# Optimization experiments

Hardware: AMD Instinct MI355X
Metric: run time of the kernel (lower is better)

Reference implementation:

```python
import jax, jax.numpy as jnp
import numpy as np

V = 128   # vocab_size
H = 1024  # rnn_hidden_size
L = 2     # rnn_num_layers
B = 64    # batch
T = 256   # seq_len


def setup_inputs() -> dict:
    key = jax.random.key(0)
    ks = jax.random.split(key, 1 + 4 * L)
    inp = {"x": jax.random.randint(ks[0], (B, T), 0, V)}
    s = 1.0 / np.sqrt(H)  # torch GRU init range
    k = 1
    for l in range(L):
        in_dim = V if l == 0 else 2 * H
        inp[f"Wih{l}"] = jax.random.uniform(ks[k], (2, 3 * H, in_dim), minval=-s, maxval=s); k += 1
        inp[f"Whh{l}"] = jax.random.uniform(ks[k], (2, 3 * H, H), minval=-s, maxval=s); k += 1
        inp[f"bih{l}"] = jax.random.uniform(ks[k], (2, 3 * H), minval=-s, maxval=s); k += 1
        inp[f"bhh{l}"] = jax.random.uniform(ks[k], (2, 3 * H), minval=-s, maxval=s); k += 1
    return inp


def _gru_dir(x_seq, Wih, Whh, bih, bhh, reverse):
    # x_seq: [B, T, in_dim]; Wih: [3H, in_dim]; Whh: [3H, H]
    xp = jnp.einsum('bti,gi->btg', x_seq, Wih) + bih  # batched input projection
    if reverse:
        xp = xp[:, ::-1]
    h0 = jnp.zeros((x_seq.shape[0], H), x_seq.dtype)

    def step(h, xpt):
        g = h @ Whh.T + bhh
        xr, xz, xn = jnp.split(xpt, 3, axis=-1)
        hr, hz, hn = jnp.split(g, 3, axis=-1)
        r = jax.nn.sigmoid(xr + hr)
        z = jax.nn.sigmoid(xz + hz)
        n = jnp.tanh(xn + r * hn)
        h_new = (1.0 - z) * n + z * h
        return h_new, h_new

    hT, ys = jax.lax.scan(step, h0, jnp.swapaxes(xp, 0, 1))  # scan over time
    ys = jnp.swapaxes(ys, 0, 1)  # [B, T, H]
    if reverse:
        ys = ys[:, ::-1]
    return ys, hT


def _encoder(x, params):
    inp_seq = jax.nn.one_hot(x, V, dtype=jnp.float32)  # [B, T, V]
    hiddens = []
    for (Wih, Whh, bih, bhh) in params:
        yf, hf = _gru_dir(inp_seq, Wih[0], Whh[0], bih[0], bhh[0], False)
        yb, hb = _gru_dir(inp_seq, Wih[1], Whh[1], bih[1], bhh[1], True)
        inp_seq = jnp.concatenate([yf, yb], axis=-1)  # [B, T, 2H]
        hiddens += [hf, hb]
    return inp_seq, jnp.stack(hiddens)  # ([B,T,2H], [2L,B,H])


def reference(x, Wih0, Whh0, bih0, bhh0, Wih1, Whh1, bih1, bhh1):
    params = [(Wih0, Whh0, bih0, bhh0), (Wih1, Whh1, bih1, bhh1)]
    return _encoder(x, params)
```

## Files before the change

### kernel.cpp

```cpp
#include <hip/hip_runtime.h>
#include <stdint.h>
#include <math.h>


#define B_  64
#define T_  256
#define H_  1024
#define G3_ 3072

#define SW_BYTES (3 * 32 * 64 * 16)
#define SX_ROW 132
#define SMEM_BYTES (SW_BYTES + 48 * SX_ROW * 4)

typedef __attribute__((ext_vector_type(8))) __bf16 bf16x8;
typedef __attribute__((ext_vector_type(4))) float  f32x4;

union FragU { uint4 u; bf16x8 b; };

__device__ __forceinline__ float bf2f(unsigned short v) {
  return __builtin_bit_cast(float, (uint32_t)v << 16);
}
__device__ __forceinline__ unsigned short f2bf(float f) {
  uint32_t u = __builtin_bit_cast(uint32_t, f);
  u += 0x7FFFu + ((u >> 16) & 1u);
  return (unsigned short)(u >> 16);
}

__device__ __forceinline__ float sigm_fast(float x) {
  x = fminf(fmaxf(x, -60.f), 60.f);
  return 1.f / (1.f + __expf(-x));
}
__device__ __forceinline__ float tanh_fast(float x) {
  const float xc = fminf(fmaxf(x, -15.f), 15.f);
  const float e = __expf(2.f * xc);
  return (e - 1.f) / (e + 1.f);
}

__device__ __forceinline__ void bar_arrive_wait(unsigned* bar, unsigned k) {
  unsigned* sub = bar + 32u * (1u + (blockIdx.x & 7u));
  bool rel = false;
  if (__hip_atomic_fetch_add(sub, 1u, __ATOMIC_RELAXED, __HIP_MEMORY_SCOPE_AGENT)
      == 16u * k - 1u) {
    if (__hip_atomic_fetch_add(bar, 1u, __ATOMIC_RELAXED, __HIP_MEMORY_SCOPE_AGENT)
        == 8u * k - 1u) {
      __hip_atomic_store(bar + 384, k, __ATOMIC_RELAXED, __HIP_MEMORY_SCOPE_AGENT);
      rel = true;
    }
  }
  if (!rel) {
    unsigned spins = 0;
    while (__hip_atomic_load(bar + 384, __ATOMIC_RELAXED, __HIP_MEMORY_SCOPE_AGENT) < k) {
      __builtin_amdgcn_s_sleep(4);
      if (++spins > (1u << 20)) break;
    }
  }
}

__global__ void detect_dtype(const unsigned short* __restrict__ p, int* __restrict__ flag) {
  const int i = threadIdx.x;
  const unsigned short v = p[2 * i];
  const int e = (v >> 7) & 0xFF;
  const unsigned long long m = __ballot(e <= 124);
  if (i == 0) *flag = (m == ~0ull) ? 1 : 0;
}

__device__ __forceinline__ float load_canon(const void* src, int i, bool isbf) {
  return isbf ? bf2f(((const unsigned short*)src)[i]) : ((const float*)src)[i];
}

__global__ void prep_split(const void* __restrict__ src, int n,
                           unsigned short* __restrict__ hi, unsigned short* __restrict__ lo,
                           const int* __restrict__ flag) {
  const int i = blockIdx.x * blockDim.x + threadIdx.x;
  if (i >= n) return;
  const bool isbf = (*flag != 0);
  const float f = load_canon(src, i, isbf);
  const unsigned short h = f2bf(f);
  hi[i] = h;
  lo[i] = f2bf(f - bf2f(h));
}

__global__ void prep_f32(const void* __restrict__ src, int n,
                         float* __restrict__ dst, const int* __restrict__ flag) {
  const int i = blockIdx.x * blockDim.x + threadIdx.x;
  if (i >= n) return;
  const bool isbf = (*flag != 0);
  dst[i] = load_canon(src, i, isbf);
}

#define LD2(K, OFF)                                                         \
  asm volatile("global_load_dwordx4 %0, %2, off offset:" OFF " sc0 sc1\n\t" \
               "global_load_dwordx4 %1, %3, off offset:" OFF " sc0 sc1"     \
               : "=&v"(ah[K].u), "=&v"(al[K].u)                             \
               : "v"(aph), "v"(apl));

#define STH(P, V)                                                 \
  asm volatile("global_store_short %0, %1, off sc0 sc1"           \
               :: "v"(P), "v"(V) : "memory");

template<int LAYER>
__global__ __launch_bounds__(128, 1) void gru_scan(
    const int*            __restrict__ x,
    const float*          __restrict__ Wih0f,
    const float*          __restrict__ bihf,
    const _Float16*       __restrict__ xp1,
    const unsigned short* __restrict__ WhhH,
    const unsigned short* __restrict__ WhhL,
    const float*          __restrict__ bhhf,
    unsigned short*       __restrict__ hhi,
    unsigned short*       __restrict__ hlo,
    unsigned short*       __restrict__ ys0_hi,
    unsigned short*       __restrict__ ys0_lo,
    void*                 __restrict__ d_out,
    const int*            __restrict__ flag,
    unsigned*             __restrict__ bar_mem)
{
  extern __shared__ unsigned char smem[];
  unsigned short* sW = (unsigned short*)smem;
  float*          sX = (float*)(smem + SW_BYTES);

  const int j0   = blockIdx.x << 4;
  const int d    = blockIdx.y;
  const int bh   = blockIdx.z;
  const int tid  = threadIdx.x;
  const int w    = tid >> 6;
  const int lane = tid & 63;
  const int quad = lane >> 4, l15 = lane & 15;
  const bool out_bf = (*flag != 0);
  const bool wlo    = (*flag == 0);

  const int j = j0 + l15;
  const size_t HF_HALF = (size_t)2 * B_ * H_;

  {
    const unsigned short* base = WhhH + (size_t)d * G3_ * H_;
    for (int idx = tid; idx < 48 * 128; idx += 128) {
      const int row = idx >> 7;
      const int c16 = idx & 127;
      const int g = row >> 4, u = row & 15;
      const int kt = c16 >> 2, q = c16 & 3;
      const uint4 v = *(const uint4*)(base + (size_t)(g * H_ + j0 + u) * H_ + (c16 << 3));
      *(uint4*)&sW[(((g << 5) + kt) << 9) + (((q << 4) + u) << 3)] = v;
    }
  }
  if (LAYER == 0) {
    const float* W0 = Wih0f + (size_t)d * G3_ * 128;
    for (int idx = tid; idx < 48 * 32; idx += 128) {
      const int row = idx >> 5, c = (idx & 31) << 2;
      const int g = row >> 4, u = row & 15;
      const float4 v = *(const float4*)(W0 + (size_t)(g * H_ + j0 + u) * 128 + c);
      *(float4*)&sX[row * SX_ROW + c] = v;
    }
  }
  __syncthreads();

  const int am = (bh << 5) + (w << 4) + l15;
  const int bb = (bh << 5) + (w << 4) + (quad << 2);
  const unsigned short *aphS[2], *aplS[2];
  unsigned short *hhiS[2], *hloS[2];
#pragma unroll
  for (int s = 0; s < 2; ++s) {
    aphS[s] = hhi + s * HF_HALF + ((size_t)d * B_ + am) * H_ + (quad << 3);
    aplS[s] = hlo + s * HF_HALF + ((size_t)d * B_ + am) * H_ + (quad << 3);
    hhiS[s] = hhi + s * HF_HALF + (size_t)d * B_ * H_;
    hloS[s] = hlo + s * HF_HALF + (size_t)d * B_ * H_;
  }

  const unsigned short* bplG[3];
#pragma unroll
  for (int g = 0; g < 3; ++g)
    bplG[g] = WhhL + (size_t)d * G3_ * H_ + (size_t)(g * H_ + j) * H_ + (quad << 3);

  const size_t dj = (size_t)d * G3_ + j;
  const float bhr = bhhf[dj];
  const float bhz = bhhf[dj + H_];
  const float bhn = bhhf[dj + 2 * H_];
  float bir = 0.f, biz = 0.f, bin_ = 0.f;
  const float *sXr = nullptr, *sXz = nullptr, *sXn = nullptr;
  if (LAYER == 0) {
    bir  = bihf[dj];
    biz  = bihf[dj + H_];
    bin_ = bihf[dj + 2 * H_];
    sXr = sX + (size_t)l15 * SX_ROW;
    sXz = sX + (size_t)(16 + l15) * SX_ROW;
    sXn = sX + (size_t)(32 + l15) * SX_ROW;
  }
  const _Float16* xpd = (LAYER == 1) ? (xp1 + (size_t)d * (B_ * T_) * G3_) : nullptr;

  float*          out_f  = (float*)d_out;
  unsigned short* out_b  = (unsigned short*)d_out;
  const size_t    HIDOFF = (size_t)B_ * T_ * 2048;

  unsigned* bar = bar_mem + (size_t)d * 1024;
  float hprev[4] = {0.f, 0.f, 0.f, 0.f};

  if (!wlo) {
    float xr[4], xz[4], xn[4];
    _Float16 xph[12];
    {
      const int te = d ? (T_ - 1) : 0;
      if (LAYER == 0) {
#pragma unroll
        for (int r = 0; r < 4; ++r) {
          const int tok = x[(bb + r) * T_ + te];
          xr[r] = sXr[tok] + bir; xz[r] = sXz[tok] + biz; xn[r] = sXn[tok] + bin_;
        }
      } else {
#pragma unroll
        for (int r = 0; r < 4; ++r) {
          const _Float16* xpb = xpd + ((size_t)(bb + r) * T_ + te) * G3_;
          xph[r * 3 + 0] = xpb[j]; xph[r * 3 + 1] = xpb[j + H_]; xph[r * 3 + 2] = xpb[j + 2 * H_];
        }
      }
    }

    for (int t = 0; t < T_; ++t) {
      const int t_eff = d ? (T_ - 1 - t) : t;
      const int pi = t & 1, po = pi ^ 1;
      const unsigned short* aph = aphS[pi];
      const unsigned short* apl = aplS[pi];

      FragU ah[32], al[32];
      LD2(0, "0")    LD2(1, "64")   LD2(2, "128")  LD2(3, "192")
      LD2(4, "256")  LD2(5, "320")  LD2(6, "384")  LD2(7, "448")
      LD2(8, "512")  LD2(9, "576")  LD2(10, "640") LD2(11, "704")
      LD2(12, "768") LD2(13, "832") LD2(14, "896") LD2(15, "960")
      LD2(16, "1024") LD2(17, "1088") LD2(18, "1152") LD2(19, "1216")
      LD2(20, "1280") LD2(21, "1344") LD2(22, "1408") LD2(23, "1472")
      LD2(24, "1536") LD2(25, "1600") LD2(26, "1664") LD2(27, "1728")
      LD2(28, "1792") LD2(29, "1856") LD2(30, "1920") LD2(31, "1984")

      f32x4 acc[3] = {};
      asm volatile("s_waitcnt vmcnt(32)" ::: "memory");
      __builtin_amdgcn_sched_barrier(0);
#pragma unroll
      for (int kt = 0; kt < 16; ++kt) {
        FragU f0, f1, f2;
        f0.u = *(const uint4*)(sW + ((kt      ) << 9) + (lane << 3));
        f1.u = *(const uint4*)(sW + ((kt +  32) << 9) + (lane << 3));
        f2.u = *(const uint4*)(sW + ((kt +  64) << 9) + (lane << 3));
        acc[0] = __builtin_amdgcn_mfma_f32_16x16x32_bf16(ah[kt].b, f0.b, acc[0], 0, 0, 0);
        acc[0] = __builtin_amdgcn_mfma_f32_16x16x32_bf16(al[kt].b, f0.b, acc[0], 0, 0, 0);
        acc[1] = __builtin_amdgcn_mfma_f32_16x16x32_bf16(ah[kt].b, f1.b, acc[1], 0, 0, 0);
        acc[1] = __builtin_amdgcn_mfma_f32_16x16x32_bf16(al[kt].b, f1.b, acc[1], 0, 0, 0);
        acc[2] = __builtin_amdgcn_mfma_f32_16x16x32_bf16(ah[kt].b, f2.b, acc[2], 0, 0, 0);
        acc[2] = __builtin_amdgcn_mfma_f32_16x16x32_bf16(al[kt].b, f2.b, acc[2], 0, 0, 0);
      }
      asm volatile("s_waitcnt vmcnt(0)" ::: "memory");
      __builtin_amdgcn_sched_barrier(0);
#pragma unroll
      for (int kt = 16; kt < 32; ++kt) {
        FragU f0, f1, f2;
        f0.u = *(const uint4*)(sW + ((kt      ) << 9) + (lane << 3));
        f1.u = *(const uint4*)(sW + ((kt +  32) << 9) + (lane << 3));
        f2.u = *(const uint4*)(sW + ((kt +  64) << 9) + (lane << 3));
        acc[0] = __builtin_amdgcn_mfma_f32_16x16x32_bf16(ah[kt].b, f0.b, acc[0], 0, 0, 0);
        acc[0] = __builtin_amdgcn_mfma_f32_16x16x32_bf16(al[kt].b, f0.b, acc[0], 0, 0, 0);
        acc[1] = __builtin_amdgcn_mfma_f32_16x16x32_bf16(ah[kt].b, f1.b, acc[1], 0, 0, 0);
        acc[1] = __builtin_amdgcn_mfma_f32_16x16x32_bf16(al[kt].b, f1.b, acc[1], 0, 0, 0);
        acc[2] = __builtin_amdgcn_mfma_f32_16x16x32_bf16(ah[kt].b, f2.b, acc[2], 0, 0, 0);
        acc[2] = __builtin_amdgcn_mfma_f32_16x16x32_bf16(al[kt].b, f2.b, acc[2], 0, 0, 0);
      }

      if (LAYER == 1) {
#pragma unroll
        for (int r = 0; r < 4; ++r) {
          xr[r] = (float)xph[r * 3 + 0];
          xz[r] = (float)xph[r * 3 + 1];
          xn[r] = (float)xph[r * 3 + 2];
        }
      }

      unsigned short* pHi = hhiS[po] + (size_t)bb * H_ + j;
      unsigned short* pLo = hloS[po] + (size_t)bb * H_ + j;
#pragma unroll
      for (int r = 0; r < 4; ++r) {
        const int b = bb + r;
        const float gr = acc[0][r] + bhr;
        const float gz = acc[1][r] + bhz;
        const float gn = acc[2][r] + bhn;
        const float rg = sigm_fast(xr[r] + gr);
        const float zg = sigm_fast(xz[r] + gz);
        const float ng = tanh_fast(xn[r] + rg * gn);
        const float hnew = (1.f - zg) * ng + zg * hprev[r];
        hprev[r] = hnew;

        const unsigned short hi = f2bf(hnew);
        const unsigned short lo = f2bf(hnew - bf2f(hi));
        STH(pHi + (size_t)r * H_, (uint32_t)hi);
        STH(pLo + (size_t)r * H_, (uint32_t)lo);

        const size_t yoff = ((size_t)b * T_ + t_eff) * 2048 + d * H_ + j;
        if (LAYER == 0) {
          ys0_hi[yoff] = hi;
          ys0_lo[yoff] = lo;
        } else {
          if (out_bf) out_b[yoff] = hi; else out_f[yoff] = hnew;
        }
        if (t == T_ - 1) {
          const size_t hh = HIDOFF + ((size_t)(LAYER * 2 + d) * B_ + b) * H_ + j;
          if (out_bf) out_b[hh] = hi; else out_f[hh] = hnew;
        }
      }

      if (t + 1 < T_) {
        asm volatile("s_waitcnt vmcnt(0)" ::: "memory");
        __syncthreads();
        const int te = d ? (T_ - 2 - t) : (t + 1);
        if (LAYER == 0) {
#pragma unroll
          for (int r = 0; r < 4; ++r) {
            const int tok = x[(bb + r) * T_ + te];
            xr[r] = sXr[tok] + bir; xz[r] = sXz[tok] + biz; xn[r] = sXn[tok] + bin_;
          }
        } else {
#pragma unroll
          for (int r = 0; r < 4; ++r) {
            const _Float16* xpb = xpd + ((size_t)(bb + r) * T_ + te) * G3_;
            xph[r * 3 + 0] = xpb[j]; xph[r * 3 + 1] = xpb[j + H_]; xph[r * 3 + 2] = xpb[j + 2 * H_];
          }
        }
        if (tid == 0) bar_arrive_wait(bar, (unsigned)(t + 1));
        __syncthreads();
      }
    }
  } else {
    for (int t = 0; t < T_; ++t) {
      const int t_eff = d ? (T_ - 1 - t) : t;
      const int pi = t & 1, po = pi ^ 1;

      float xr[4], xz[4], xn[4];
      if (LAYER == 0) {
#pragma unroll
        for (int r = 0; r < 4; ++r) {
          const int tok = x[(bb + r) * T_ + t_eff];
          xr[r] = sXr[tok] + bir; xz[r] = sXz[tok] + biz; xn[r] = sXn[tok] + bin_;
        }
      } else {
#pragma unroll
        for (int r = 0; r < 4; ++r) {
          const _Float16* xpb = xpd + ((size_t)(bb + r) * T_ + t_eff) * G3_;
          xr[r] = (float)xpb[j]; xz[r] = (float)xpb[j + H_]; xn[r] = (float)xpb[j + 2 * H_];
        }
      }

      const unsigned short* aph = aphS[pi];
      const unsigned short* apl = aplS[pi];
      f32x4 acc[3] = {};
#pragma unroll
      for (int kt = 0; kt < 32; ++kt) {
        FragU ah, al;
        ah.u = *(const uint4*)(aph + (kt << 5));
        al.u = *(const uint4*)(apl + (kt << 5));
#pragma unroll
        for (int g = 0; g < 3; ++g) {
          FragU fb, fl;
          fb.u = *(const uint4*)(sW + (((g << 5) + kt) << 9) + (lane << 3));
          fl.u = *(const uint4*)(bplG[g] + (kt << 5));
          acc[g] = __builtin_amdgcn_mfma_f32_16x16x32_bf16(ah.b, fb.b, acc[g], 0, 0, 0);
          acc[g] = __builtin_amdgcn_mfma_f32_16x16x32_bf16(al.b, fb.b, acc[g], 0, 0, 0);
          acc[g] = __builtin_amdgcn_mfma_f32_16x16x32_bf16(ah.b, fl.b, acc[g], 0, 0, 0);
        }
      }

#pragma unroll
      for (int r = 0; r < 4; ++r) {
        const int b = bb + r;
        const float gr = acc[0][r] + bhr;
        const float gz = acc[1][r] + bhz;
        const float gn = acc[2][r] + bhn;
        const float rg = 1.f / (1.f + expf(-(xr[r] + gr)));
        const float zg = 1.f / (1.f + expf(-(xz[r] + gz)));
        const float ng = tanhf(xn[r] + rg * gn);
        const float hnew = (1.f - zg) * ng + zg * hprev[r];
        hprev[r] = hnew;

        const size_t ho = (size_t)b * H_ + j;
        const unsigned short hi = f2bf(hnew);
        const unsigned short lo = f2bf(hnew - bf2f(hi));
        hhiS[po][ho] = hi;
        hloS[po][ho] = lo;

        const size_t yoff = ((size_t)b * T_ + t_eff) * 2048 + d * H_ + j;
        if (LAYER == 0) {
          ys0_hi[yoff] = hi;
          ys0_lo[yoff] = lo;
        } else {
          if (out_bf) out_b[yoff] = hi; else out_f[yoff] = hnew;
        }
        if (t == T_ - 1) {
          const size_t hh = HIDOFF + ((size_t)(LAYER * 2 + d) * B_ + b) * H_ + j;
          if (out_bf) out_b[hh] = hi; else out_f[hh] = hnew;
        }
      }

      if (t + 1 < T_) {
        __syncthreads();
        if (tid == 0) {
          __builtin_amdgcn_fence(__ATOMIC_RELEASE, "agent");
          bar_arrive_wait(bar, (unsigned)(t + 1));
          __builtin_amdgcn_fence(__ATOMIC_ACQUIRE, "agent");
        }
        __syncthreads();
      }
    }
  }
}

__global__ __launch_bounds__(256) void xp1_gemm(
    const unsigned short* __restrict__ Ahi,
    const unsigned short* __restrict__ Alo,
    const unsigned short* __restrict__ Bhi,
    const unsigned short* __restrict__ Blo,
    const float*          __restrict__ biasf,
    _Float16*             __restrict__ xp1,
    const int*            __restrict__ flag)
{
  const int nt  = blockIdx.x;
  const int mt  = blockIdx.y;
  const int d   = blockIdx.z;
  const int tid = threadIdx.x;
  const int w = tid >> 6, lane = tid & 63;
  const int quad = lane >> 4, l15 = lane & 15;
  const int wm = w >> 1, wn = w & 1;
  const bool wlo = (*flag == 0);

  __shared__ unsigned short sAh[128][40];
  __shared__ unsigned short sAl[128][40];
  __shared__ unsigned short sBh[128][40];
  __shared__ unsigned short sBl[128][40];

  const int srow = tid >> 1;
  const int scol = (tid & 1) << 4;
  const unsigned short* gAh = Ahi + (size_t)(mt * 128 + srow) * 2048 + scol;
  const unsigned short* gAl = Alo + (size_t)(mt * 128 + srow) * 2048 + scol;
  const unsigned short* gBh = Bhi + (size_t)d * G3_ * 2048
                                  + (size_t)(nt * 128 + srow) * 2048 + scol;
  const unsigned short* gBl = Blo + (size_t)d * G3_ * 2048
                                  + (size_t)(nt * 128 + srow) * 2048 + scol;

  f32x4 acc[4][4] = {};

  for (int k0 = 0; k0 < 2048; k0 += 32) {
    const uint4 a0 = *(const uint4*)(gAh + k0);
    const uint4 a1 = *(const uint4*)(gAh + k0 + 8);
    const uint4 l0 = *(const uint4*)(gAl + k0);
    const uint4 l1 = *(const uint4*)(gAl + k0 + 8);
    const uint4 b0 = *(const uint4*)(gBh + k0);
    const uint4 b1 = *(const uint4*)(gBh + k0 + 8);
    uint4 c0, c1;
    if (wlo) { c0 = *(const uint4*)(gBl + k0); c1 = *(const uint4*)(gBl + k0 + 8); }
    __syncthreads();
    *(uint4*)&sAh[srow][scol]     = a0;
    *(uint4*)&sAh[srow][scol + 8] = a1;
    *(uint4*)&sAl[srow][scol]     = l0;
    *(uint4*)&sAl[srow][scol + 8] = l1;
    *(uint4*)&sBh[srow][scol]     = b0;
    *(uint4*)&sBh[srow][scol + 8] = b1;
    if (wlo) {
      *(uint4*)&sBl[srow][scol]     = c0;
      *(uint4*)&sBl[srow][scol + 8] = c1;
    }
    __syncthreads();

    bf16x8 fah[4], fal[4], fbh[4];
#pragma unroll
    for (int i = 0; i < 4; ++i) {
      FragU fa; fa.u = *(const uint4*)&sAh[(wm << 6) + (i << 4) + l15][quad << 3]; fah[i] = fa.b;
      FragU fl; fl.u = *(const uint4*)&sAl[(wm << 6) + (i << 4) + l15][quad << 3]; fal[i] = fl.b;
      FragU fb; fb.u = *(const uint4*)&sBh[(wn << 6) + (i << 4) + l15][quad << 3]; fbh[i] = fb.b;
    }
#pragma unroll
    for (int i = 0; i < 4; ++i)
#pragma unroll
      for (int jj = 0; jj < 4; ++jj) {
        acc[i][jj] = __builtin_amdgcn_mfma_f32_16x16x32_bf16(fah[i], fbh[jj], acc[i][jj], 0, 0, 0);
        acc[i][jj] = __builtin_amdgcn_mfma_f32_16x16x32_bf16(fal[i], fbh[jj], acc[i][jj], 0, 0, 0);
      }
    if (wlo) {
#pragma unroll
      for (int jj = 0; jj < 4; ++jj) {
        FragU fc; fc.u = *(const uint4*)&sBl[(wn << 6) + (jj << 4) + l15][quad << 3];
#pragma unroll
        for (int i = 0; i < 4; ++i)
          acc[i][jj] = __builtin_amdgcn_mfma_f32_16x16x32_bf16(fah[i], fc.b, acc[i][jj], 0, 0, 0);
      }
    }
  }

#pragma unroll
  for (int jj = 0; jj < 4; ++jj) {
    const int col = nt * 128 + (wn << 6) + (jj << 4) + l15;
    const float bias = biasf[(size_t)d * G3_ + col];
#pragma unroll
    for (int i = 0; i < 4; ++i) {
      const int m = mt * 128 + (wm << 6) + (i << 4) + (quad << 2);
      _Float16* op = xp1 + ((size_t)d * (B_ * T_) + m) * G3_ + col;
#pragma unroll
      for (int r = 0; r < 4; ++r) op[(size_t)r * G3_] = (_Float16)(acc[i][jj][r] + bias);
    }
  }
}

extern "C" void kernel_launch(void* const* d_in, const int* in_sizes, int n_in,
                              void* d_out, int out_size, void* d_ws, size_t ws_size,
                              hipStream_t stream)
{
  const int*  x    = (const int*)d_in[0];
  const void* Wih0 = d_in[1];
  const void* Whh0 = d_in[2];
  const void* bih0 = d_in[3];
  const void* bhh0 = d_in[4];
  const void* Wih1 = d_in[5];
  const void* Whh1 = d_in[6];
  const void* bih1 = d_in[7];
  const void* bhh1 = d_in[8];

  const size_t FLAG_B = 256;
  const size_t XP1_B  = (size_t)2 * B_ * T_ * G3_ * 2;
  const size_t YS_B   = (size_t)B_ * T_ * 2048 * 2;
  const size_t WHH_B  = (size_t)2 * G3_ * H_ * 2;
  const size_t WIH1_B = (size_t)2 * G3_ * 2048 * 2;
  const size_t WIH0_B = (size_t)2 * G3_ * 128 * 4;
  const size_t BIAS_B = (size_t)2 * G3_ * 4;
  const size_t HB_B   = (size_t)2 * 2 * B_ * H_ * 2;
  const size_t BAR_B  = 8192;
  const size_t NEED = FLAG_B + XP1_B + 2 * YS_B + 4 * WHH_B + 2 * WIH1_B
                    + WIH0_B + 4 * BIAS_B + 2 * HB_B + BAR_B;
  if (ws_size < NEED) return;

  char* p = (char*)d_ws;
  int*            flag    = (int*)p;            p += FLAG_B;
  _Float16*       xp1     = (_Float16*)p;       p += XP1_B;
  unsigned short* ys0_hi  = (unsigned short*)p; p += YS_B;
  unsigned short* ys0_lo  = (unsigned short*)p; p += YS_B;
  unsigned short* Whh0H   = (unsigned short*)p; p += WHH_B;
  unsigned short* Whh0L   = (unsigned short*)p; p += WHH_B;
  unsigned short* Whh1H   = (unsigned short*)p; p += WHH_B;
  unsigned short* Whh1L   = (unsigned short*)p; p += WHH_B;
  unsigned short* Wih1H   = (unsigned short*)p; p += WIH1_B;
  unsigned short* Wih1L   = (unsigned short*)p; p += WIH1_B;
  float*          Wih0f   = (float*)p;          p += WIH0_B;
  float*          bih0f   = (float*)p;          p += BIAS_B;
  float*          bhh0f   = (float*)p;          p += BIAS_B;
  float*          bih1f   = (float*)p;          p += BIAS_B;
  float*          bhh1f   = (float*)p;          p += BIAS_B;
  char*           hbase   = p;
  unsigned short* hhi     = (unsigned short*)hbase;
  unsigned short* hlo     = (unsigned short*)(hbase + HB_B);
  unsigned*       bar     = (unsigned*)(hbase + 2 * HB_B);

  hipFuncSetAttribute((const void*)&gru_scan<0>,
                      hipFuncAttributeMaxDynamicSharedMemorySize, SMEM_BYTES);
  hipFuncSetAttribute((const void*)&gru_scan<1>,
                      hipFuncAttributeMaxDynamicSharedMemorySize, SMEM_BYTES);

  detect_dtype<<<1, 64, 0, stream>>>((const unsigned short*)bih0, flag);

  const int NWHH  = 2 * G3_ * H_;
  const int NWIH1 = 2 * G3_ * 2048;
  const int NWIH0 = 2 * G3_ * 128;
  const int NBIAS = 2 * G3_;
  prep_split<<<(NWHH  + 255) / 256, 256, 0, stream>>>(Whh0, NWHH,  Whh0H, Whh0L, flag);
  prep_split<<<(NWHH  + 255) / 256, 256, 0, stream>>>(Whh1, NWHH,  Whh1H, Whh1L, flag);
  prep_split<<<(NWIH1 + 255) / 256, 256, 0, stream>>>(Wih1, NWIH1, Wih1H, Wih1L, flag);
  prep_f32<<<(NWIH0 + 255) / 256, 256, 0, stream>>>(Wih0, NWIH0, Wih0f, flag);
  prep_f32<<<(NBIAS + 255) / 256, 256, 0, stream>>>(bih0, NBIAS, bih0f, flag);
  prep_f32<<<(NBIAS + 255) / 256, 256, 0, stream>>>(bhh0, NBIAS, bhh0f, flag);
  prep_f32<<<(NBIAS + 255) / 256, 256, 0, stream>>>(bih1, NBIAS, bih1f, flag);
  prep_f32<<<(NBIAS + 255) / 256, 256, 0, stream>>>(bhh1, NBIAS, bhh1f, flag);

  hipMemsetAsync(hbase, 0, 2 * HB_B + BAR_B, stream);
  gru_scan<0><<<dim3(64, 2, 2), 128, SMEM_BYTES, stream>>>(
      x, Wih0f, bih0f, nullptr, Whh0H, Whh0L, bhh0f,
      hhi, hlo, ys0_hi, ys0_lo, d_out, flag, bar);

  xp1_gemm<<<dim3(24, 128, 2), 256, 0, stream>>>(ys0_hi, ys0_lo, Wih1H, Wih1L, bih1f, xp1, flag);

  hipMemsetAsync(hbase, 0, 2 * HB_B + BAR_B, stream);
  gru_scan<1><<<dim3(64, 2, 2), 128, SMEM_BYTES, stream>>>(
      x, nullptr, nullptr, xp1, Whh1H, Whh1L, bhh1f,
      hhi, hlo, nullptr, nullptr, d_out, flag, bar);
}
```

Baseline: 12.49 ms.

## Replace atomic counter barrier with per-group flag barrier and pack hidden hi/lo words

Replaces the per-direction two-level atomic fetch-add barrier with a flag-based barrier. Each block publishes its step count to a padded flag, a leader block ballots over all 64 flags and then releases per-group go flags, and barriers are now scoped per (direction, batch-half) group rather than per direction. The hidden state's bf16 hi and lo parts are interleaved into one 32-bit word, so each element is one dword store and one load stream instead of two, with perm instructions unpacking them before the MFMAs. It also moves the layer-0 token-embedding lookup after the matmul so the token load overlaps the barrier. This adds a leader hop and larger barrier memory, and the polling latency of the leader could dominate.

```diff
diff --git a/kernel.cpp b/kernel.cpp
--- a/kernel.cpp
+++ b/kernel.cpp
@@ -36,24 +36,16 @@
   return (e - 1.f) / (e + 1.f);
 }
 
-__device__ __forceinline__ void bar_arrive_wait(unsigned* bar, unsigned k) {
-  unsigned* sub = bar + 32u * (1u + (blockIdx.x & 7u));
-  bool rel = false;
-  if (__hip_atomic_fetch_add(sub, 1u, __ATOMIC_RELAXED, __HIP_MEMORY_SCOPE_AGENT)
-      == 16u * k - 1u) {
-    if (__hip_atomic_fetch_add(bar, 1u, __ATOMIC_RELAXED, __HIP_MEMORY_SCOPE_AGENT)
-        == 8u * k - 1u) {
-      __hip_atomic_store(bar + 384, k, __ATOMIC_RELAXED, __HIP_MEMORY_SCOPE_AGENT);
-      rel = true;
-    }
-  }
-  if (!rel) {
-    unsigned spins = 0;
-    while (__hip_atomic_load(bar + 384, __ATOMIC_RELAXED, __HIP_MEMORY_SCOPE_AGENT) < k) {
-      __builtin_amdgcn_s_sleep(4);
-      if (++spins > (1u << 20)) break;
-    }
-  }
+__device__ __forceinline__ void unpack2(const FragU& q0, const FragU& q1,
+                                        FragU& ah, FragU& al) {
+  ah.u.x = __builtin_amdgcn_perm(q0.u.y, q0.u.x, 0x05040100u);
+  ah.u.y = __builtin_amdgcn_perm(q0.u.w, q0.u.z, 0x05040100u);
+  ah.u.z = __builtin_amdgcn_perm(q1.u.y, q1.u.x, 0x05040100u);
+  ah.u.w = __builtin_amdgcn_perm(q1.u.w, q1.u.z, 0x05040100u);
+  al.u.x = __builtin_amdgcn_perm(q0.u.y, q0.u.x, 0x07060302u);
+  al.u.y = __builtin_amdgcn_perm(q0.u.w, q0.u.z, 0x07060302u);
+  al.u.z = __builtin_amdgcn_perm(q1.u.y, q1.u.x, 0x07060302u);
+  al.u.w = __builtin_amdgcn_perm(q1.u.w, q1.u.z, 0x07060302u);
 }
 
 __global__ void detect_dtype(const unsigned short* __restrict__ p, int* __restrict__ flag) {
@@ -88,14 +80,14 @@
   dst[i] = load_canon(src, i, isbf);
 }
 
-#define LD2(K, OFF)                                                         \
-  asm volatile("global_load_dwordx4 %0, %2, off offset:" OFF " sc0 sc1\n\t" \
-               "global_load_dwordx4 %1, %3, off offset:" OFF " sc0 sc1"     \
-               : "=&v"(ah[K].u), "=&v"(al[K].u)                             \
-               : "v"(aph), "v"(apl));
-
-#define STH(P, V)                                                 \
-  asm volatile("global_store_short %0, %1, off sc0 sc1"           \
+#define LDP(K, O0, O1)                                                      \
+  asm volatile("global_load_dwordx4 %0, %2, off offset:" O0 " sc0 sc1\n\t"  \
+               "global_load_dwordx4 %1, %2, off offset:" O1 " sc0 sc1"      \
+               : "=&v"(p0[K].u), "=&v"(p1[K].u)                             \
+               : "v"(ap32));
+
+#define STW(P, V)                                                 \
+  asm volatile("global_store_dword %0, %1, off sc0 sc1"           \
                :: "v"(P), "v"(V) : "memory");
 
 template<int LAYER>
@@ -107,8 +99,7 @@
     const unsigned short* __restrict__ WhhH,
     const unsigned short* __restrict__ WhhL,
     const float*          __restrict__ bhhf,
-    unsigned short*       __restrict__ hhi,
-    unsigned short*       __restrict__ hlo,
+    unsigned*             __restrict__ h32,
     unsigned short*       __restrict__ ys0_hi,
     unsigned short*       __restrict__ ys0_lo,
     void*                 __restrict__ d_out,
@@ -128,6 +119,7 @@
   const int quad = lane >> 4, l15 = lane & 15;
   const bool out_bf = (*flag != 0);
   const bool wlo    = (*flag == 0);
+  const bool leader = (blockIdx.x == 0);
 
   const int j = j0 + l15;
   const size_t HF_HALF = (size_t)2 * B_ * H_;
@@ -156,14 +148,12 @@
 
   const int am = (bh << 5) + (w << 4) + l15;
   const int bb = (bh << 5) + (w << 4) + (quad << 2);
-  const unsigned short *aphS[2], *aplS[2];
-  unsigned short *hhiS[2], *hloS[2];
+  const unsigned *ap32S[2];
+  unsigned *h32S[2];
 #pragma unroll
   for (int s = 0; s < 2; ++s) {
-    aphS[s] = hhi + s * HF_HALF + ((size_t)d * B_ + am) * H_ + (quad << 3);
-    aplS[s] = hlo + s * HF_HALF + ((size_t)d * B_ + am) * H_ + (quad << 3);
-    hhiS[s] = hhi + s * HF_HALF + (size_t)d * B_ * H_;
-    hloS[s] = hlo + s * HF_HALF + (size_t)d * B_ * H_;
+    ap32S[s] = h32 + s * HF_HALF + ((size_t)d * B_ + am) * H_ + (quad << 3);
+    h32S[s]  = h32 + s * HF_HALF + (size_t)d * B_ * H_;
   }
 
   const unsigned short* bplG[3];
@@ -191,20 +181,17 @@
   unsigned short* out_b  = (unsigned short*)d_out;
   const size_t    HIDOFF = (size_t)B_ * T_ * 2048;
 
-  unsigned* bar = bar_mem + (size_t)d * 1024;
+  unsigned* grp = bar_mem + (size_t)(d * 2 + bh) * 72 * 1024;
   float hprev[4] = {0.f, 0.f, 0.f, 0.f};
 
   if (!wlo) {
-    float xr[4], xz[4], xn[4];
+    int ptok[4];
     _Float16 xph[12];
     {
       const int te = d ? (T_ - 1) : 0;
       if (LAYER == 0) {
 #pragma unroll
-        for (int r = 0; r < 4; ++r) {
-          const int tok = x[(bb + r) * T_ + te];
-          xr[r] = sXr[tok] + bir; xz[r] = sXz[tok] + biz; xn[r] = sXn[tok] + bin_;
-        }
+        for (int r = 0; r < 4; ++r) ptok[r] = x[(bb + r) * T_ + te];
       } else {
 #pragma unroll
         for (int r = 0; r < 4; ++r) {
@@ -217,52 +204,63 @@
     for (int t = 0; t < T_; ++t) {
       const int t_eff = d ? (T_ - 1 - t) : t;
       const int pi = t & 1, po = pi ^ 1;
-      const unsigned short* aph = aphS[pi];
-      const unsigned short* apl = aplS[pi];
-
-      FragU ah[32], al[32];
-      LD2(0, "0")    LD2(1, "64")   LD2(2, "128")  LD2(3, "192")
-      LD2(4, "256")  LD2(5, "320")  LD2(6, "384")  LD2(7, "448")
-      LD2(8, "512")  LD2(9, "576")  LD2(10, "640") LD2(11, "704")
-      LD2(12, "768") LD2(13, "832") LD2(14, "896") LD2(15, "960")
-      LD2(16, "1024") LD2(17, "1088") LD2(18, "1152") LD2(19, "1216")
-      LD2(20, "1280") LD2(21, "1344") LD2(22, "1408") LD2(23, "1472")
-      LD2(24, "1536") LD2(25, "1600") LD2(26, "1664") LD2(27, "1728")
-      LD2(28, "1792") LD2(29, "1856") LD2(30, "1920") LD2(31, "1984")
+      const unsigned* ap32 = ap32S[pi];
+
+      FragU p0[32], p1[32];
+      LDP(0, "0", "16")        LDP(1, "128", "144")    LDP(2, "256", "272")
+      LDP(3, "384", "400")     LDP(4, "512", "528")    LDP(5, "640", "656")
+      LDP(6, "768", "784")     LDP(7, "896", "912")    LDP(8, "1024", "1040")
+      LDP(9, "1152", "1168")   LDP(10, "1280", "1296") LDP(11, "1408", "1424")
+      LDP(12, "1536", "1552")  LDP(13, "1664", "1680") LDP(14, "1792", "1808")
+      LDP(15, "1920", "1936")  LDP(16, "2048", "2064") LDP(17, "2176", "2192")
+      LDP(18, "2304", "2320")  LDP(19, "2432", "2448") LDP(20, "2560", "2576")
+      LDP(21, "2688", "2704")  LDP(22, "2816", "2832") LDP(23, "2944", "2960")
+      LDP(24, "3072", "3088")  LDP(25, "3200", "3216") LDP(26, "3328", "3344")
+      LDP(27, "3456", "3472")  LDP(28, "3584", "3600") LDP(29, "3712", "3728")
+      LDP(30, "3840", "3856")  LDP(31, "3968", "3984")
 
       f32x4 acc[3] = {};
       asm volatile("s_waitcnt vmcnt(32)" ::: "memory");
       __builtin_amdgcn_sched_barrier(0);
 #pragma unroll
       for (int kt = 0; kt < 16; ++kt) {
-        FragU f0, f1, f2;
+        FragU ah, al, f0, f1, f2;
+        unpack2(p0[kt], p1[kt], ah, al);
         f0.u = *(const uint4*)(sW + ((kt      ) << 9) + (lane << 3));
         f1.u = *(const uint4*)(sW + ((kt +  32) << 9) + (lane << 3));
         f2.u = *(const uint4*)(sW + ((kt +  64) << 9) + (lane << 3));
-        acc[0] = __builtin_amdgcn_mfma_f32_16x16x32_bf16(ah[kt].b, f0.b, acc[0], 0, 0, 0);
-        acc[0] = __builtin_amdgcn_mfma_f32_16x16x32_bf16(al[kt].b, f0.b, acc[0], 0, 0, 0);
-        acc[1] = __builtin_amdgcn_mfma_f32_16x16x32_bf16(ah[kt].b, f1.b, acc[1], 0, 0, 0);
-        acc[1] = __builtin_amdgcn_mfma_f32_16x16x32_bf16(al[kt].b, f1.b, acc[1], 0, 0, 0);
-        acc[2] = __builtin_amdgcn_mfma_f32_16x16x32_bf16(ah[kt].b, f2.b, acc[2], 0, 0, 0);
-        acc[2] = __builtin_amdgcn_mfma_f32_16x16x32_bf16(al[kt].b, f2.b, acc[2], 0, 0, 0);
+        acc[0] = __builtin_amdgcn_mfma_f32_16x16x32_bf16(ah.b, f0.b, acc[0], 0, 0, 0);
+        acc[0] = __builtin_amdgcn_mfma_f32_16x16x32_bf16(al.b, f0.b, acc[0], 0, 0, 0);
+        acc[1] = __builtin_amdgcn_mfma_f32_16x16x32_bf16(ah.b, f1.b, acc[1], 0, 0, 0);
+        acc[1] = __builtin_amdgcn_mfma_f32_16x16x32_bf16(al.b, f1.b, acc[1], 0, 0, 0);
+        acc[2] = __builtin_amdgcn_mfma_f32_16x16x32_bf16(ah.b, f2.b, acc[2], 0, 0, 0);
+        acc[2] = __builtin_amdgcn_mfma_f32_16x16x32_bf16(al.b, f2.b, acc[2], 0, 0, 0);
       }
       asm volatile("s_waitcnt vmcnt(0)" ::: "memory");
       __builtin_amdgcn_sched_barrier(0);
 #pragma unroll
       for (int kt = 16; kt < 32; ++kt) {
-        FragU f0, f1, f2;
+        FragU ah, al, f0, f1, f2;
+        unpack2(p0[kt], p1[kt], ah, al);
         f0.u = *(const uint4*)(sW + ((kt      ) << 9) + (lane << 3));
         f1.u = *(const uint4*)(sW + ((kt +  32) << 9) + (lane << 3));
         f2.u = *(const uint4*)(sW + ((kt +  64) << 9) + (lane << 3));
-        acc[0] = __builtin_amdgcn_mfma_f32_16x16x32_bf16(ah[kt].b, f0.b, acc[0], 0, 0, 0);
-        acc[0] = __builtin_amdgcn_mfma_f32_16x16x32_bf16(al[kt].b, f0.b, acc[0], 0, 0, 0);
-        acc[1] = __builtin_amdgcn_mfma_f32_16x16x32_bf16(ah[kt].b, f1.b, acc[1], 0, 0, 0);
-        acc[1] = __builtin_amdgcn_mfma_f32_16x16x32_bf16(al[kt].b, f1.b, acc[1], 0, 0, 0);
-        acc[2] = __builtin_amdgcn_mfma_f32_16x16x32_bf16(ah[kt].b, f2.b, acc[2], 0, 0, 0);
-        acc[2] = __builtin_amdgcn_mfma_f32_16x16x32_bf16(al[kt].b, f2.b, acc[2], 0, 0, 0);
-      }
-
-      if (LAYER == 1) {
+        acc[0] = __builtin_amdgcn_mfma_f32_16x16x32_bf16(ah.b, f0.b, acc[0], 0, 0, 0);
+        acc[0] = __builtin_amdgcn_mfma_f32_16x16x32_bf16(al.b, f0.b, acc[0], 0, 0, 0);
+        acc[1] = __builtin_amdgcn_mfma_f32_16x16x32_bf16(ah.b, f1.b, acc[1], 0, 0, 0);
+        acc[1] = __builtin_amdgcn_mfma_f32_16x16x32_bf16(al.b, f1.b, acc[1], 0, 0, 0);
+        acc[2] = __builtin_amdgcn_mfma_f32_16x16x32_bf16(ah.b, f2.b, acc[2], 0, 0, 0);
+        acc[2] = __builtin_amdgcn_mfma_f32_16x16x32_bf16(al.b, f2.b, acc[2], 0, 0, 0);
+      }
+
+      float xr[4], xz[4], xn[4];
+      if (LAYER == 0) {
+#pragma unroll
+        for (int r = 0; r < 4; ++r) {
+          const int tok = ptok[r];
+          xr[r] = sXr[tok] + bir; xz[r] = sXz[tok] + biz; xn[r] = sXn[tok] + bin_;
+        }
+      } else {
 #pragma unroll
         for (int r = 0; r < 4; ++r) {
           xr[r] = (float)xph[r * 3 + 0];
@@ -271,8 +269,7 @@
         }
       }
 
-      unsigned short* pHi = hhiS[po] + (size_t)bb * H_ + j;
-      unsigned short* pLo = hloS[po] + (size_t)bb * H_ + j;
+      unsigned* pW = h32S[po] + (size_t)bb * H_ + j;
 #pragma unroll
       for (int r = 0; r < 4; ++r) {
         const int b = bb + r;
@@ -287,8 +284,8 @@
 
         const unsigned short hi = f2bf(hnew);
         const unsigned short lo = f2bf(hnew - bf2f(hi));
-        STH(pHi + (size_t)r * H_, (uint32_t)hi);
-        STH(pLo + (size_t)r * H_, (uint32_t)lo);
+        const unsigned hv = (unsigned)hi | ((unsigned)lo << 16);
+        STW(pW + (size_t)r * H_, hv);
 
         const size_t yoff = ((size_t)b * T_ + t_eff) * 2048 + d * H_ + j;
         if (LAYER == 0) {
@@ -304,15 +301,16 @@
       }
 
       if (t + 1 < T_) {
+        const unsigned k = (unsigned)(t + 1);
         asm volatile("s_waitcnt vmcnt(0)" ::: "memory");
         __syncthreads();
+        if (tid == 0)
+          __hip_atomic_store(grp + (unsigned)blockIdx.x * 1024u, k,
+                             __ATOMIC_RELAXED, __HIP_MEMORY_SCOPE_AGENT);
         const int te = d ? (T_ - 2 - t) : (t + 1);
         if (LAYER == 0) {
 #pragma unroll
-          for (int r = 0; r < 4; ++r) {
-            const int tok = x[(bb + r) * T_ + te];
-            xr[r] = sXr[tok] + bir; xz[r] = sXz[tok] + biz; xn[r] = sXn[tok] + bin_;
-          }
+          for (int r = 0; r < 4; ++r) ptok[r] = x[(bb + r) * T_ + te];
         } else {
 #pragma unroll
           for (int r = 0; r < 4; ++r) {
@@ -320,7 +318,29 @@
             xph[r * 3 + 0] = xpb[j]; xph[r * 3 + 1] = xpb[j + H_]; xph[r * 3 + 2] = xpb[j + 2 * H_];
           }
         }
-        if (tid == 0) bar_arrive_wait(bar, (unsigned)(t + 1));
+        if (leader) {
+          if (tid < 64) {
+            unsigned* fl = grp + (unsigned)tid * 1024u;
+            unsigned spins = 0;
+            for (;;) {
+              const unsigned v = __hip_atomic_load(fl, __ATOMIC_RELAXED, __HIP_MEMORY_SCOPE_AGENT);
+              if (__ballot(v >= k) == ~0ull) break;
+              __builtin_amdgcn_s_sleep(1);
+              if (++spins > (1u << 20)) break;
+            }
+            if (tid < 8)
+              __hip_atomic_store(grp + (64u + (unsigned)tid) * 1024u, k,
+                                 __ATOMIC_RELAXED, __HIP_MEMORY_SCOPE_AGENT);
+          }
+        } else if (tid == 0) {
+          unsigned* gl = grp + (64u + ((unsigned)blockIdx.x & 7u)) * 1024u;
+          unsigned spins = 0;
+          while (__hip_atomic_load(gl, __ATOMIC_RELAXED, __HIP_MEMORY_SCOPE_AGENT) < k) {
+            if (spins < 8) __builtin_amdgcn_s_sleep(1);
+            else           __builtin_amdgcn_s_sleep(8);
+            if (++spins > (1u << 20)) break;
+          }
+        }
         __syncthreads();
       }
     }
@@ -344,14 +364,14 @@
         }
       }
 
-      const unsigned short* aph = aphS[pi];
-      const unsigned short* apl = aplS[pi];
+      const unsigned* ap32 = ap32S[pi];
       f32x4 acc[3] = {};
 #pragma unroll
       for (int kt = 0; kt < 32; ++kt) {
-        FragU ah, al;
-        ah.u = *(const uint4*)(aph + (kt << 5));
-        al.u = *(const uint4*)(apl + (kt << 5));
+        FragU q0, q1, ah, al;
+        q0.u = *(const uint4*)(ap32 + (kt << 5));
+        q1.u = *(const uint4*)(ap32 + (kt << 5) + 4);
+        unpack2(q0, q1, ah, al);
 #pragma unroll
         for (int g = 0; g < 3; ++g) {
           FragU fb, fl;
@@ -363,6 +383,7 @@
         }
       }
 
+      unsigned* pW = h32S[po] + (size_t)bb * H_ + j;
 #pragma unroll
       for (int r = 0; r < 4; ++r) {
         const int b = bb + r;
@@ -375,11 +396,9 @@
         const float hnew = (1.f - zg) * ng + zg * hprev[r];
         hprev[r] = hnew;
 
-        const size_t ho = (size_t)b * H_ + j;
         const unsigned short hi = f2bf(hnew);
         const unsigned short lo = f2bf(hnew - bf2f(hi));
-        hhiS[po][ho] = hi;
-        hloS[po][ho] = lo;
+        pW[(size_t)r * H_] = (unsigned)hi | ((unsigned)lo << 16);
 
         const size_t yoff = ((size_t)b * T_ + t_eff) * 2048 + d * H_ + j;
         if (LAYER == 0) {
@@ -395,12 +414,37 @@
       }
 
       if (t + 1 < T_) {
+        const unsigned k = (unsigned)(t + 1);
         __syncthreads();
         if (tid == 0) {
           __builtin_amdgcn_fence(__ATOMIC_RELEASE, "agent");
-          bar_arrive_wait(bar, (unsigned)(t + 1));
-          __builtin_amdgcn_fence(__ATOMIC_ACQUIRE, "agent");
-        }
+          __hip_atomic_store(grp + (unsigned)blockIdx.x * 1024u, k,
+                             __ATOMIC_RELAXED, __HIP_MEMORY_SCOPE_AGENT);
+        }
+        if (leader) {
+          if (tid < 64) {
+            unsigned* fl = grp + (unsigned)tid * 1024u;
+            unsigned spins = 0;
+            for (;;) {
+              const unsigned v = __hip_atomic_load(fl, __ATOMIC_RELAXED, __HIP_MEMORY_SCOPE_AGENT);
+              if (__ballot(v >= k) == ~0ull) break;
+              __builtin_amdgcn_s_sleep(4);
+              if (++spins > (1u << 20)) break;
+            }
+            if (tid < 8)
+              __hip_atomic_store(grp + (64u + (unsigned)tid) * 1024u, k,
+                                 __ATOMIC_RELAXED, __HIP_MEMORY_SCOPE_AGENT);
+          }
+        } else if (tid == 0) {
+          unsigned* gl = grp + (64u + ((unsigned)blockIdx.x & 7u)) * 1024u;
+          unsigned spins = 0;
+          while (__hip_atomic_load(gl, __ATOMIC_RELAXED, __HIP_MEMORY_SCOPE_AGENT) < k) {
+            if (spins < 8) __builtin_amdgcn_s_sleep(1);
+            else           __builtin_amdgcn_s_sleep(8);
+            if (++spins > (1u << 20)) break;
+          }
+        }
+        if (tid == 0) __builtin_amdgcn_fence(__ATOMIC_ACQUIRE, "agent");
         __syncthreads();
       }
     }
@@ -523,10 +567,10 @@
   const size_t WIH1_B = (size_t)2 * G3_ * 2048 * 2;
   const size_t WIH0_B = (size_t)2 * G3_ * 128 * 4;
   const size_t BIAS_B = (size_t)2 * G3_ * 4;
-  const size_t HB_B   = (size_t)2 * 2 * B_ * H_ * 2;
-  const size_t BAR_B  = 8192;
+  const size_t HW_B   = (size_t)2 * 2 * B_ * H_ * 4;
+  const size_t BAR_B  = (size_t)4 * 72 * 4096;
   const size_t NEED = FLAG_B + XP1_B + 2 * YS_B + 4 * WHH_B + 2 * WIH1_B
-                    + WIH0_B + 4 * BIAS_B + 2 * HB_B + BAR_B;
+                    + WIH0_B + 4 * BIAS_B + HW_B + BAR_B;
   if (ws_size < NEED) return;
 
   char* p = (char*)d_ws;
@@ -546,14 +590,13 @@
   float*          bih1f   = (float*)p;          p += BIAS_B;
   float*          bhh1f   = (float*)p;          p += BIAS_B;
   char*           hbase   = p;
-  unsigned short* hhi     = (unsigned short*)hbase;
-  unsigned short* hlo     = (unsigned short*)(hbase + HB_B);
-  unsigned*       bar     = (unsigned*)(hbase + 2 * HB_B);
-
-  hipFuncSetAttribute((const void*)&gru_scan<0>,
-                      hipFuncAttributeMaxDynamicSharedMemorySize, SMEM_BYTES);
-  hipFuncSetAttribute((const void*)&gru_scan<1>,
-                      hipFuncAttributeMaxDynamicSharedMemorySize, SMEM_BYTES);
+  unsigned*       h32     = (unsigned*)hbase;
+  unsigned*       bar     = (unsigned*)(hbase + HW_B);
+
+  (void)hipFuncSetAttribute((const void*)&gru_scan<0>,
+                            hipFuncAttributeMaxDynamicSharedMemorySize, SMEM_BYTES);
+  (void)hipFuncSetAttribute((const void*)&gru_scan<1>,
+                            hipFuncAttributeMaxDynamicSharedMemorySize, SMEM_BYTES);
 
   detect_dtype<<<1, 64, 0, stream>>>((const unsigned short*)bih0, flag);
 
@@ -570,15 +613,15 @@
   prep_f32<<<(NBIAS + 255) / 256, 256, 0, stream>>>(bih1, NBIAS, bih1f, flag);
   prep_f32<<<(NBIAS + 255) / 256, 256, 0, stream>>>(bhh1, NBIAS, bhh1f, flag);
 
-  hipMemsetAsync(hbase, 0, 2 * HB_B + BAR_B, stream);
+  (void)hipMemsetAsync(hbase, 0, HW_B + BAR_B, stream);
   gru_scan<0><<<dim3(64, 2, 2), 128, SMEM_BYTES, stream>>>(
       x, Wih0f, bih0f, nullptr, Whh0H, Whh0L, bhh0f,
-      hhi, hlo, ys0_hi, ys0_lo, d_out, flag, bar);
+      h32, ys0_hi, ys0_lo, d_out, flag, bar);
 
   xp1_gemm<<<dim3(24, 128, 2), 256, 0, stream>>>(ys0_hi, ys0_lo, Wih1H, Wih1L, bih1f, xp1, flag);
 
-  hipMemsetAsync(hbase, 0, 2 * HB_B + BAR_B, stream);
+  (void)hipMemsetAsync(hbase, 0, HW_B + BAR_B, stream);
   gru_scan<1><<<dim3(64, 2, 2), 128, SMEM_BYTES, stream>>>(
       x, nullptr, nullptr, xp1, Whh1H, Whh1L, bhh1f,
-      hhi, hlo, nullptr, nullptr, d_out, flag, bar);
-}
+      h32, nullptr, nullptr, d_out, flag, bar);
+}
```

New measurement: 14.35 ms. 1.15x slower.
